# Performance work log

Hardware: AMD Instinct MI355X
Metric: run time of the kernel (lower is better)

## Reference

```python
import jax, jax.numpy as jnp
import numpy as np


def setup_inputs() -> dict:
    key = jax.random.key(0)
    k1, k2, k3 = jax.random.split(key, 3)
    B, L = 32, 1024
    inp = jax.random.normal(k1, (B, L, L), dtype=jnp.float32)
    mask = jax.random.randint(k2, (B, L), 0, 2).astype(jnp.int32)
    tgt = jax.random.normal(k3, (B, L, L), dtype=jnp.float32)
    return {"input": inp, "input_mask": mask, "target": tgt}


def reference(input, input_mask, target):
    # input, target: (B, L, L); input_mask: (B, L) 0/1
    B, L, _ = input.shape
    lens = input_mask.sum(axis=-1) - 2  # raw_sent_len per sample, (B,)
    # Align: target[i,:n,:n] vs input[i,1:1+n,1:1+n]**2, with n <= L-1.
    A = input[:, 1:, 1:] ** 2          # (B, L-1, L-1)
    T = target[:, : L - 1, : L - 1]    # (B, L-1, L-1)
    idx = jnp.arange(L - 1)
    m = (idx[None, :] < lens[:, None]).astype(input.dtype)  # (B, L-1)
    m2 = m[:, :, None] * m[:, None, :]                       # (B, L-1, L-1)
    per_sum = jnp.sum(jnp.abs(T - A) * m2, axis=(1, 2))      # (B,)
    denom = jnp.maximum(lens * lens, 1).astype(input.dtype)
    per_mean = jnp.where(lens > 0, per_sum / denom, jnp.zeros((), input.dtype))
    return per_mean.sum() / B
```

## Files before the change

### kernel.cpp

```cpp
#include <hip/hip_runtime.h>

#define L 1024
#define NB 32
#define ROWS 8
#define NCHUNK 128

__global__ void prep_kernel(const int* __restrict__ mask,
                            float* __restrict__ scale,
                            int* __restrict__ lens_out) {
    const int b = blockIdx.x;
    const int t = threadIdx.x;
    const int* mrow = mask + b * L;
    int s = 0;
    for (int j = t; j < L; j += 256) s += mrow[j];
    for (int off = 32; off > 0; off >>= 1) s += __shfl_down(s, off, 64);
    __shared__ int wsum[4];
    if ((t & 63) == 0) wsum[t >> 6] = s;
    __syncthreads();
    if (t == 0) {
        const int total = wsum[0] + wsum[1] + wsum[2] + wsum[3];
        const int lens = total - 2;
        lens_out[b] = lens;
        float sc = 0.0f;
        if (lens > 0) {
            const float d = (float)lens * (float)lens;
            sc = 1.0f / (32.0f * d);
        }
        scale[b] = sc;
    }
}

__global__ void __launch_bounds__(256)
loss_kernel(const float* __restrict__ input,
            const float* __restrict__ target,
            const float* __restrict__ scale,
            const int* __restrict__ lens,
            float* __restrict__ partials) {
    const int b = blockIdx.x;
    const int chunk = blockIdx.y;
    const int len = lens[b];
    const int row0 = chunk * ROWS;
    const int t = threadIdx.x;

    float acc = 0.0f;
    if (row0 < len) {
        const int rend = min(row0 + ROWS, len);
        const size_t slab = (size_t)b * L * L;
        for (int i = row0; i < rend; ++i) {
            const float* trow = target + slab + (size_t)i * L;
            const float* irow = input  + slab + (size_t)(i + 1) * L + 1;
            for (int j = t * 4; j < len; j += 1024) {
                const float4 tv = *reinterpret_cast<const float4*>(trow + j);
                const float a0 = irow[j + 0];
                const float a1 = irow[j + 1];
                const float a2 = irow[j + 2];
                const float a3 = irow[j + 3];
                if (j + 3 < len) {
                    acc += fabsf(tv.x - a0 * a0) + fabsf(tv.y - a1 * a1)
                         + fabsf(tv.z - a2 * a2) + fabsf(tv.w - a3 * a3);
                } else {
                    const float tvv[4] = {tv.x, tv.y, tv.z, tv.w};
                    const float avv[4] = {a0, a1, a2, a3};
                    for (int k = 0; k < 4; ++k)
                        if (j + k < len) acc += fabsf(tvv[k] - avv[k] * avv[k]);
                }
            }
        }
    }

    for (int off = 32; off > 0; off >>= 1) acc += __shfl_down(acc, off, 64);
    __shared__ float wsum[4];
    if ((t & 63) == 0) wsum[t >> 6] = acc;
    __syncthreads();
    if (t == 0) {
        const float s = wsum[0] + wsum[1] + wsum[2] + wsum[3];
        partials[b * NCHUNK + chunk] = s * scale[b];
    }
}

__global__ void __launch_bounds__(256)
reduce_kernel(const float* __restrict__ partials, float* __restrict__ out) {
    const int t = threadIdx.x;
    float s = 0.0f;
    for (int k = t; k < NB * NCHUNK; k += 256) s += partials[k];
    for (int off = 32; off > 0; off >>= 1) s += __shfl_down(s, off, 64);
    __shared__ float wsum[4];
    if ((t & 63) == 0) wsum[t >> 6] = s;
    __syncthreads();
    if (t == 0) out[0] = wsum[0] + wsum[1] + wsum[2] + wsum[3];
}

extern "C" void kernel_launch(void* const* d_in, const int* in_sizes, int n_in,
                              void* d_out, int out_size, void* d_ws, size_t ws_size,
                              hipStream_t stream) {
    const float* input  = (const float*)d_in[0];
    const int*   mask   = (const int*)d_in[1];
    const float* target = (const float*)d_in[2];
    float* out = (float*)d_out;

    float* scale    = (float*)d_ws;
    int*   lens     = (int*)((char*)d_ws + 32 * sizeof(float));
    float* partials = (float*)((char*)d_ws + 64 * sizeof(float));

    prep_kernel<<<dim3(NB), dim3(256), 0, stream>>>(mask, scale, lens);
    loss_kernel<<<dim3(NB, NCHUNK), dim3(256), 0, stream>>>(input, target, scale, lens, partials);
    reduce_kernel<<<dim3(1), dim3(256), 0, stream>>>(partials, out);
}
```

Before: 249.8 us.

## Use aligned float4 input loads, two rows per block, and a grid-stride over row chunks

The input row is now read as an aligned float4 plus one extra scalar and shifted in registers, replacing four unaligned scalar loads. Each 256-thread block now handles two rows at once, 512 columns per half-block with a second pass at column offset 512. The grid shrinks from 128 to 32 blocks in y, and each block strides over 16-row chunks with an unrolled inner loop, so more loads are in flight per thread. Fewer blocks could reduce occupancy and parallelism for this memory-bound pass, and the extra scalar load reads one element past the quad.

After: 250.0 us. No clear change (+0.0%).

```diff
diff --git a/kernel.cpp b/kernel.cpp
--- a/kernel.cpp
+++ b/kernel.cpp
@@ -2,8 +2,9 @@
 
 #define L 1024
 #define NB 32
-#define ROWS 8
-#define NCHUNK 128
+#define GRIDY 32
+#define CHROWS 16
+#define NPART (NB * GRIDY)
 
 __global__ void prep_kernel(const int* __restrict__ mask,
                             float* __restrict__ scale,
@@ -22,12 +23,27 @@
         const int lens = total - 2;
         lens_out[b] = lens;
         float sc = 0.0f;
-        if (lens > 0) {
-            const float d = (float)lens * (float)lens;
-            sc = 1.0f / (32.0f * d);
-        }
+        if (lens > 0) sc = 1.0f / (32.0f * (float)lens * (float)lens);
         scale[b] = sc;
     }
+}
+
+__device__ __forceinline__ float quad_contrib(const float* __restrict__ trow,
+                                              const float* __restrict__ irow,
+                                              int j, int len) {
+    const float4 tv = *reinterpret_cast<const float4*>(trow + j);
+    const float4 iv = *reinterpret_cast<const float4*>(irow + j);
+    const float nx = irow[j + 4];
+    const float c0 = fabsf(tv.x - iv.y * iv.y);
+    const float c1 = fabsf(tv.y - iv.z * iv.z);
+    const float c2 = fabsf(tv.z - iv.w * iv.w);
+    const float c3 = fabsf(tv.w - nx * nx);
+    if (j + 4 <= len) return c0 + c1 + c2 + c3;
+    float r = 0.0f;
+    if (j + 0 < len) r += c0;
+    if (j + 1 < len) r += c1;
+    if (j + 2 < len) r += c2;
+    return r;
 }
 
 __global__ void __launch_bounds__(256)
@@ -37,33 +53,28 @@
             const int* __restrict__ lens,
             float* __restrict__ partials) {
     const int b = blockIdx.x;
-    const int chunk = blockIdx.y;
     const int len = lens[b];
-    const int row0 = chunk * ROWS;
     const int t = threadIdx.x;
+    const int rsel = t >> 7;
+    const int j0 = (t & 127) * 4;
+
+    const size_t slab = (size_t)b * L * L;
+    const float* __restrict__ tg = target + slab;
+    const float* __restrict__ in = input + slab;
 
     float acc = 0.0f;
-    if (row0 < len) {
-        const int rend = min(row0 + ROWS, len);
-        const size_t slab = (size_t)b * L * L;
-        for (int i = row0; i < rend; ++i) {
-            const float* trow = target + slab + (size_t)i * L;
-            const float* irow = input  + slab + (size_t)(i + 1) * L + 1;
-            for (int j = t * 4; j < len; j += 1024) {
-                const float4 tv = *reinterpret_cast<const float4*>(trow + j);
-                const float a0 = irow[j + 0];
-                const float a1 = irow[j + 1];
-                const float a2 = irow[j + 2];
-                const float a3 = irow[j + 3];
-                if (j + 3 < len) {
-                    acc += fabsf(tv.x - a0 * a0) + fabsf(tv.y - a1 * a1)
-                         + fabsf(tv.z - a2 * a2) + fabsf(tv.w - a3 * a3);
-                } else {
-                    const float tvv[4] = {tv.x, tv.y, tv.z, tv.w};
-                    const float avv[4] = {a0, a1, a2, a3};
-                    for (int k = 0; k < 4; ++k)
-                        if (j + k < len) acc += fabsf(tvv[k] - avv[k] * avv[k]);
-                }
+
+    for (int c = blockIdx.y; c * CHROWS < len; c += GRIDY) {
+        const int base = c * CHROWS;
+#pragma unroll
+        for (int s = 0; s < CHROWS / 2; ++s) {
+            const int i = base + 2 * s + rsel;
+            if (i < len && j0 < len) {
+                const float* trow = tg + (size_t)i * L;
+                const float* irow = in + (size_t)(i + 1) * L;
+                acc += quad_contrib(trow, irow, j0, len);
+                const int j1 = j0 + 512;
+                if (j1 < len) acc += quad_contrib(trow, irow, j1, len);
             }
         }
     }
@@ -73,8 +84,7 @@
     if ((t & 63) == 0) wsum[t >> 6] = acc;
     __syncthreads();
     if (t == 0) {
-        const float s = wsum[0] + wsum[1] + wsum[2] + wsum[3];
-        partials[b * NCHUNK + chunk] = s * scale[b];
+        partials[b * GRIDY + blockIdx.y] = (wsum[0] + wsum[1] + wsum[2] + wsum[3]) * scale[b];
     }
 }
 
@@ -82,7 +92,7 @@
 reduce_kernel(const float* __restrict__ partials, float* __restrict__ out) {
     const int t = threadIdx.x;
     float s = 0.0f;
-    for (int k = t; k < NB * NCHUNK; k += 256) s += partials[k];
+    for (int k = t; k < NPART; k += 256) s += partials[k];
     for (int off = 32; off > 0; off >>= 1) s += __shfl_down(s, off, 64);
     __shared__ float wsum[4];
     if ((t & 63) == 0) wsum[t >> 6] = s;
@@ -103,6 +113,6 @@
     float* partials = (float*)((char*)d_ws + 64 * sizeof(float));
 
     prep_kernel<<<dim3(NB), dim3(256), 0, stream>>>(mask, scale, lens);
-    loss_kernel<<<dim3(NB, NCHUNK), dim3(256), 0, stream>>>(input, target, scale, lens, partials);
+    loss_kernel<<<dim3(NB, GRIDY), dim3(256), 0, stream>>>(input, target, scale, lens, partials);
     reduce_kernel<<<dim3(1), dim3(256), 0, stream>>>(partials, out);
 }
```
